# Kernel tuning notes

Hardware: AMD Instinct MI355X
Metric: run time of the kernel (lower is better)

Reference implementation:

```python
import jax, jax.numpy as jnp
import numpy as np

N_NODES = 100000
N_EDGES = 3200000
IN_DIM, HID_DIM, N_CLASS = 64, 32, 20


def setup_inputs() -> dict:
    key = jax.random.key(0)
    k1, k2, k3, k4, k5, k6 = jax.random.split(key, 6)
    x = jax.random.normal(k1, (N_NODES, IN_DIM), dtype=jnp.float32)
    edge_index = jax.random.randint(k2, (2, N_EDGES), 0, N_NODES, dtype=jnp.int64)
    W1 = jax.random.normal(k3, (IN_DIM, HID_DIM), dtype=jnp.float32) / np.sqrt(IN_DIM)
    b1 = jnp.zeros((HID_DIM,), dtype=jnp.float32)
    Wout = jax.random.normal(k4, (HID_DIM, N_CLASS), dtype=jnp.float32) / np.sqrt(HID_DIM)
    bout = jnp.zeros((N_CLASS,), dtype=jnp.float32)
    return {"x": x, "edge_index": edge_index, "W1": W1, "b1": b1, "Wout": Wout, "bout": bout}


def gcn_conv(x, edge_index, W, b):
    # PyG GCNConv defaults: add self-loops, symmetric deg^{-1/2} normalization.
    n = x.shape[0]
    loop = jnp.arange(n, dtype=edge_index.dtype)
    row = jnp.concatenate([edge_index[0], loop])  # source
    col = jnp.concatenate([edge_index[1], loop])  # target
    deg = jax.ops.segment_sum(jnp.ones_like(col, dtype=x.dtype), col, num_segments=n)
    dis = jnp.where(deg > 0, deg ** -0.5, 0.0)
    norm = dis[row] * dis[col]  # [E+N]
    xw = x @ W  # [N, HID]
    msg = norm[:, None] * xw[row]  # [E+N, HID]
    agg = jax.ops.segment_sum(msg, col, num_segments=n)
    return agg + b


def reference(x, edge_index, W1, b1, Wout, bout):
    h = gcn_conv(x, edge_index, W1, b1)
    emb = jax.nn.relu(h)
    return emb @ Wout + bout
```

## Files before the change

kernel.cpp:

```cpp
#include <hip/hip_runtime.h>
#include <hip/hip_fp16.h>
#include <math.h>

#define N_NODES 100000
#define N_EDGES 3200000
#define IN_DIM 64
#define HID_DIM 32
#define N_CLASS 20

#define BKT_BITS 6
#define BKT_W    64
#define NBKT     1563
#define CAP_BKT  2560
#define ENT_R    (CAP_BKT / 512)

#define SUP_SHIFT 12
#define SUP_W    (1 << SUP_SHIFT)
#define NS       25
#define CAP_S    132000
#define CH1      2048
#define NBLK1    ((N_EDGES + CH1 - 1) / CH1)
#define CH2      4096
#define BPS      ((CAP_S + CH2 - 1) / CH2)

__device__ __forceinline__ int get_idx(const int* __restrict__ ei32, int wide, int pos) {
    return wide ? ei32[2 * (long long)pos] : ei32[pos];
}

__global__ void __launch_bounds__(512, 4)
kS1(const int* __restrict__ ei32, int* __restrict__ scursor, unsigned int* __restrict__ sp) {
    __shared__ int lh[NS], lgb[NS], lrt[NS];
    __shared__ int sAny;
    if (threadIdx.x == 0) sAny = 0;
    if (threadIdx.x < NS) { lh[threadIdx.x] = 0; lrt[threadIdx.x] = 0; }
    int base = blockIdx.x * CH1;
    int e0 = base + (int)threadIdx.x;
    int probe = (e0 < N_EDGES) ? ei32[2 * (long long)e0 + 1] : 0;
    __syncthreads();
    if (probe) sAny = 1;
    __syncthreads();
    int wide = (sAny == 0);

    int src[4], dst[4];
#pragma unroll
    for (int k = 0; k < 4; ++k) {
        int e = base + k * 512 + (int)threadIdx.x;
        if (e < N_EDGES) {
            src[k] = get_idx(ei32, wide, e);
            dst[k] = get_idx(ei32, wide, N_EDGES + e);
            atomicAdd(&lh[dst[k] >> SUP_SHIFT], 1);
        } else dst[k] = -1;
    }
    __syncthreads();
    if (threadIdx.x < NS && lh[threadIdx.x])
        lgb[threadIdx.x] = atomicAdd(&scursor[threadIdx.x], lh[threadIdx.x]);
    __syncthreads();
#pragma unroll
    for (int k = 0; k < 4; ++k) {
        if (dst[k] >= 0) {
            int s = dst[k] >> SUP_SHIFT;
            int r = atomicAdd(&lrt[s], 1);
            int rel = lgb[s] + r;
            if (rel < CAP_S)
                sp[(size_t)s * CAP_S + rel] = ((unsigned)src[k] << SUP_SHIFT) |
                                              (unsigned)(dst[k] & (SUP_W - 1));
        }
    }
}

__global__ void __launch_bounds__(512, 4)
kS2(const unsigned int* __restrict__ sp, const int* __restrict__ scursor,
    int* __restrict__ gcursor, unsigned int* __restrict__ pk, int* __restrict__ deg) {
    __shared__ int lh[BKT_W], lgb[BKT_W], lrt[BKT_W];
    __shared__ int ndeg[SUP_W];
    int s = blockIdx.x / BPS;
    int j = blockIdx.x % BPS;
    int sbase = s * CAP_S;
    int scount = min(scursor[s], CAP_S);
    int start = j * CH2;
    if (start >= scount) return;
    int end = min(start + CH2, scount);
    for (int i = threadIdx.x; i < SUP_W; i += 512) ndeg[i] = 0;
    if (threadIdx.x < BKT_W) { lh[threadIdx.x] = 0; lrt[threadIdx.x] = 0; }
    __syncthreads();
    unsigned ent[8]; int fb[8];
#pragma unroll
    for (int k = 0; k < 8; ++k) {
        int i = start + k * 512 + (int)threadIdx.x;
        if (i < end) {
            ent[k] = sp[sbase + i];
            int ld = (int)(ent[k] & (SUP_W - 1));
            fb[k] = ld >> BKT_BITS;
            atomicAdd(&lh[fb[k]], 1);
            atomicAdd(&ndeg[ld], 1);
        } else fb[k] = -1;
    }
    __syncthreads();
    if (threadIdx.x < BKT_W && lh[threadIdx.x]) {
        int b = s * BKT_W + (int)threadIdx.x;
        if (b < NBKT) lgb[threadIdx.x] = atomicAdd(&gcursor[b], lh[threadIdx.x]);
    }
    __syncthreads();
#pragma unroll
    for (int k = 0; k < 8; ++k) {
        if (fb[k] >= 0) {
            int b = s * BKT_W + fb[k];
            int r = atomicAdd(&lrt[fb[k]], 1);
            int rel = lgb[fb[k]] + r;
            if (rel < CAP_BKT)
                pk[(size_t)b * CAP_BKT + rel] =
                    ((ent[k] >> SUP_SHIFT) << BKT_BITS) | (ent[k] & (BKT_W - 1));
        }
    }
    __syncthreads();
    int nodebase = s << SUP_SHIFT;
    for (int i = threadIdx.x; i < SUP_W; i += 512) {
        int c = ndeg[i];
        if (c && nodebase + i < N_NODES) atomicAdd(&deg[nodebase + i], c);
    }
}

__global__ void k_xw(const float* __restrict__ x, const float* __restrict__ W1,
                     const int* __restrict__ deg, __half* __restrict__ xw16) {
    __shared__ float sW[IN_DIM * HID_DIM];
    for (int i = threadIdx.x; i < IN_DIM * HID_DIM; i += blockDim.x) sW[i] = W1[i];
    __syncthreads();
    int tid = blockIdx.x * blockDim.x + threadIdx.x;
    int node = tid >> 3;
    int q = tid & 7;
    if (node >= N_NODES) return;
    const float4* xr = reinterpret_cast<const float4*>(x + (size_t)node * IN_DIM);
    float4 a = make_float4(0.f, 0.f, 0.f, 0.f);
#pragma unroll
    for (int k4 = 0; k4 < IN_DIM / 4; ++k4) {
        float4 xv = xr[k4];
        const float4 w0 = *reinterpret_cast<const float4*>(&sW[(k4 * 4 + 0) * HID_DIM + q * 4]);
        const float4 w1 = *reinterpret_cast<const float4*>(&sW[(k4 * 4 + 1) * HID_DIM + q * 4]);
        const float4 w2 = *reinterpret_cast<const float4*>(&sW[(k4 * 4 + 2) * HID_DIM + q * 4]);
        const float4 w3 = *reinterpret_cast<const float4*>(&sW[(k4 * 4 + 3) * HID_DIM + q * 4]);
        a.x += xv.x * w0.x + xv.y * w1.x + xv.z * w2.x + xv.w * w3.x;
        a.y += xv.x * w0.y + xv.y * w1.y + xv.z * w2.y + xv.w * w3.y;
        a.z += xv.x * w0.z + xv.y * w1.z + xv.z * w2.z + xv.w * w3.z;
        a.w += xv.x * w0.w + xv.y * w1.w + xv.z * w2.w + xv.w * w3.w;
    }
    float d = rsqrtf((float)(deg[node] + 1));
    union { __half2 h2[2]; uint2 u; } cvt;
    cvt.h2[0] = __floats2half2_rn(a.x * d, a.y * d);
    cvt.h2[1] = __floats2half2_rn(a.z * d, a.w * d);
    *reinterpret_cast<uint2*>(xw16 + (size_t)node * HID_DIM + q * 4) = cvt.u;
}

__device__ __forceinline__ void acc_row(float4& acc, uint2 u) {
    union U { unsigned u; __half2 hh; };
    U a0; a0.u = u.x; U a1; a1.u = u.y;
    float2 f0 = __half22float2(a0.hh);
    float2 f1 = __half22float2(a1.hh);
    acc.x += f0.x; acc.y += f0.y; acc.z += f1.x; acc.w += f1.y;
}

__global__ void __launch_bounds__(512, 8)
kD_gather(const unsigned int* __restrict__ pk, const int* __restrict__ gcursor,
          const int* __restrict__ deg, const __half* __restrict__ xw16,
          const float* __restrict__ b1, const float* __restrict__ Wout,
          const float* __restrict__ bout, float* __restrict__ out) {
    __shared__ int   ssrc[CAP_BKT];
    __shared__ int   lcnt[BKT_W], lstart[BKT_W], lrt[BKT_W];
    __shared__ float sW[HID_DIM * N_CLASS];
    __shared__ float sb1[HID_DIM];
    __shared__ float sbo[N_CLASS];
    for (int i = threadIdx.x; i < HID_DIM * N_CLASS; i += blockDim.x) sW[i] = Wout[i];
    if (threadIdx.x < HID_DIM) sb1[threadIdx.x] = b1[threadIdx.x];
    if (threadIdx.x < N_CLASS) sbo[threadIdx.x] = bout[threadIdx.x];
    if (threadIdx.x < BKT_W) lrt[threadIdx.x] = 0;
    int b = blockIdx.x;
    size_t gb = (size_t)b * CAP_BKT;
    int bsz = min(gcursor[b], CAP_BKT);
    if (threadIdx.x < BKT_W) {
        int node = b * BKT_W + (int)threadIdx.x;
        int v = (node < N_NODES) ? deg[node] : 0;
        lcnt[threadIdx.x] = v;
        int s = v;
#pragma unroll
        for (int d = 1; d < BKT_W; d <<= 1) {
            int t = __shfl_up(s, d, BKT_W);
            if ((int)threadIdx.x >= d) s += t;
        }
        lstart[threadIdx.x] = s - v;
    }
    __syncthreads();
    unsigned ents[ENT_R];
#pragma unroll
    for (int i = 0; i < ENT_R; ++i) {
        int idx = i * 512 + (int)threadIdx.x;
        ents[i] = (idx < bsz) ? pk[gb + idx] : 0xFFFFFFFFu;
    }
#pragma unroll
    for (int i = 0; i < ENT_R; ++i) {
        if (ents[i] != 0xFFFFFFFFu) {
            int ld = (int)(ents[i] & (BKT_W - 1));
            int r = atomicAdd(&lrt[ld], 1);
            int pos = lstart[ld] + r;
            if (pos < CAP_BKT) ssrc[pos] = (int)(ents[i] >> BKT_BITS);
        }
    }
    __syncthreads();

    int grp = threadIdx.x >> 3, part = threadIdx.x & 7;
    int node = b * BKT_W + grp;
    if (node >= N_NODES) return;

    float4 acc = make_float4(0.f, 0.f, 0.f, 0.f);
    acc_row(acc, *reinterpret_cast<const uint2*>(xw16 + (size_t)node * HID_DIM + part * 4));
    float dc = rsqrtf((float)(lcnt[grp] + 1));

    {
        int e = lstart[grp], end = min(lstart[grp] + lcnt[grp], CAP_BKT);
        while (e + 8 <= end) {
            uint2 us[8];
#pragma unroll
            for (int j = 0; j < 8; ++j)
                us[j] = *reinterpret_cast<const uint2*>(xw16 + (size_t)ssrc[e + j] * HID_DIM + part * 4);
#pragma unroll
            for (int j = 0; j < 8; ++j) acc_row(acc, us[j]);
            e += 8;
        }
        for (; e < end; ++e)
            acc_row(acc, *reinterpret_cast<const uint2*>(xw16 + (size_t)ssrc[e] * HID_DIM + part * 4));
    }
    float e0 = fmaxf(dc * acc.x + sb1[part * 4 + 0], 0.f);
    float e1 = fmaxf(dc * acc.y + sb1[part * 4 + 1], 0.f);
    float e2 = fmaxf(dc * acc.z + sb1[part * 4 + 2], 0.f);
    float e3 = fmaxf(dc * acc.w + sb1[part * 4 + 3], 0.f);
    float o[N_CLASS];
#pragma unroll
    for (int cl = 0; cl < N_CLASS; ++cl) {
        o[cl] = e0 * sW[(part * 4 + 0) * N_CLASS + cl]
              + e1 * sW[(part * 4 + 1) * N_CLASS + cl]
              + e2 * sW[(part * 4 + 2) * N_CLASS + cl]
              + e3 * sW[(part * 4 + 3) * N_CLASS + cl];
    }
#pragma unroll
    for (int m = 1; m < 8; m <<= 1) {
#pragma unroll
        for (int cl = 0; cl < N_CLASS; ++cl) o[cl] += __shfl_xor(o[cl], m, 64);
    }
    if (part < 5) {
        float4 w = make_float4(o[part * 4 + 0] + sbo[part * 4 + 0],
                               o[part * 4 + 1] + sbo[part * 4 + 1],
                               o[part * 4 + 2] + sbo[part * 4 + 2],
                               o[part * 4 + 3] + sbo[part * 4 + 3]);
        *reinterpret_cast<float4*>(out + (size_t)node * N_CLASS + part * 4) = w;
    }
}

extern "C" void kernel_launch(void* const* d_in, const int* in_sizes, int n_in,
                              void* d_out, int out_size, void* d_ws, size_t ws_size,
                              hipStream_t stream) {
    const float* x    = (const float*)d_in[0];
    const int*   ei32 = (const int*)d_in[1];
    const float* W1   = (const float*)d_in[2];
    const float* b1   = (const float*)d_in[3];
    const float* Wout = (const float*)d_in[4];
    const float* bout = (const float*)d_in[5];
    float* out = (float*)d_out;

    unsigned int* sp      = (unsigned int*)d_ws;
    __half*       xw16    = (__half*)d_ws;
    unsigned int* pk      = sp + (size_t)NS * CAP_S;
    int*          gcursor = (int*)(pk + (size_t)NBKT * CAP_BKT);
    int*          scursor = gcursor + NBKT;
    int*          deg     = scursor + NS;

    hipMemsetAsync(gcursor, 0, (size_t)(NBKT + NS + N_NODES) * sizeof(int), stream);

    kS1<<<NBLK1, 512, 0, stream>>>(ei32, scursor, sp);
    kS2<<<NS * BPS, 512, 0, stream>>>(sp, scursor, gcursor, pk, deg);
    k_xw<<<(N_NODES * 8 + 255) / 256, 256, 0, stream>>>(x, W1, deg, xw16);
    kD_gather<<<NBKT, 512, 0, stream>>>(pk, gcursor, deg, xw16, b1, Wout, bout, out);
}
```

Before: 128.1 us.

## Split fp16 XW into two 16-column slices and halve edge lists per lane group

The fp16 XW table is stored as two separate 16-column arrays, each 3.2 MB instead of one 6.4 MB array, so each gather pass works over a smaller footprint that fits caches better. Each node's 8 lanes are split into two halves that each process half the neighbor list over one slice, then combine with a shuffle, and the kernel makes two passes, one per slice. Bucket-entry loads and output stores use nontemporal hints. In exchange, every source index is read twice from LDS, and the row segments fetched per edge are narrower.

Measured after the change: 139.2 us. 1.09x slower.

```diff
diff --git a/kernel.cpp b/kernel.cpp
--- a/kernel.cpp
+++ b/kernel.cpp
@@ -7,6 +7,7 @@
 #define IN_DIM 64
 #define HID_DIM 32
 #define N_CLASS 20
+#define SLICE 16
 
 #define BKT_BITS 6
 #define BKT_W    64
@@ -121,7 +122,8 @@
 }
 
 __global__ void k_xw(const float* __restrict__ x, const float* __restrict__ W1,
-                     const int* __restrict__ deg, __half* __restrict__ xw16) {
+                     const int* __restrict__ deg, __half* __restrict__ xwA,
+                     __half* __restrict__ xwB) {
     __shared__ float sW[IN_DIM * HID_DIM];
     for (int i = threadIdx.x; i < IN_DIM * HID_DIM; i += blockDim.x) sW[i] = W1[i];
     __syncthreads();
@@ -147,7 +149,9 @@
     union { __half2 h2[2]; uint2 u; } cvt;
     cvt.h2[0] = __floats2half2_rn(a.x * d, a.y * d);
     cvt.h2[1] = __floats2half2_rn(a.z * d, a.w * d);
-    *reinterpret_cast<uint2*>(xw16 + (size_t)node * HID_DIM + q * 4) = cvt.u;
+    __half* dst = (q < 4) ? (xwA + (size_t)node * SLICE + q * 4)
+                          : (xwB + (size_t)node * SLICE + (q - 4) * 4);
+    *reinterpret_cast<uint2*>(dst) = cvt.u;
 }
 
 __device__ __forceinline__ void acc_row(float4& acc, uint2 u) {
@@ -158,11 +162,31 @@
     acc.x += f0.x; acc.y += f0.y; acc.z += f1.x; acc.w += f1.y;
 }
 
+__device__ __forceinline__ float4 gather_slice(const __half* __restrict__ xws,
+                                               const int* __restrict__ ssrc,
+                                               int beg, int end, int p) {
+    float4 acc = make_float4(0.f, 0.f, 0.f, 0.f);
+    int e = beg;
+    while (e + 8 <= end) {
+        uint2 us[8];
+#pragma unroll
+        for (int j = 0; j < 8; ++j)
+            us[j] = *reinterpret_cast<const uint2*>(xws + (size_t)ssrc[e + j] * SLICE + p * 4);
+#pragma unroll
+        for (int j = 0; j < 8; ++j) acc_row(acc, us[j]);
+        e += 8;
+    }
+    for (; e < end; ++e)
+        acc_row(acc, *reinterpret_cast<const uint2*>(xws + (size_t)ssrc[e] * SLICE + p * 4));
+    return acc;
+}
+
 __global__ void __launch_bounds__(512, 8)
 kD_gather(const unsigned int* __restrict__ pk, const int* __restrict__ gcursor,
-          const int* __restrict__ deg, const __half* __restrict__ xw16,
-          const float* __restrict__ b1, const float* __restrict__ Wout,
-          const float* __restrict__ bout, float* __restrict__ out) {
+          const int* __restrict__ deg, const __half* __restrict__ xwA,
+          const __half* __restrict__ xwB, const float* __restrict__ b1,
+          const float* __restrict__ Wout, const float* __restrict__ bout,
+          float* __restrict__ out) {
     __shared__ int   ssrc[CAP_BKT];
     __shared__ int   lcnt[BKT_W], lstart[BKT_W], lrt[BKT_W];
     __shared__ float sW[HID_DIM * N_CLASS];
@@ -192,7 +216,7 @@
 #pragma unroll
     for (int i = 0; i < ENT_R; ++i) {
         int idx = i * 512 + (int)threadIdx.x;
-        ents[i] = (idx < bsz) ? pk[gb + idx] : 0xFFFFFFFFu;
+        ents[i] = (idx < bsz) ? __builtin_nontemporal_load(pk + gb + idx) : 0xFFFFFFFFu;
     }
 #pragma unroll
     for (int i = 0; i < ENT_R; ++i) {
@@ -205,51 +229,60 @@
     }
     __syncthreads();
 
-    int grp = threadIdx.x >> 3, part = threadIdx.x & 7;
+    int grp = threadIdx.x >> 3;
+    int part = threadIdx.x & 7;
+    int p = part & 3;
+    int h = part >> 2;
     int node = b * BKT_W + grp;
     if (node >= N_NODES) return;
 
-    float4 acc = make_float4(0.f, 0.f, 0.f, 0.f);
-    acc_row(acc, *reinterpret_cast<const uint2*>(xw16 + (size_t)node * HID_DIM + part * 4));
-    float dc = rsqrtf((float)(lcnt[grp] + 1));
-
-    {
-        int e = lstart[grp], end = min(lstart[grp] + lcnt[grp], CAP_BKT);
-        while (e + 8 <= end) {
-            uint2 us[8];
-#pragma unroll
-            for (int j = 0; j < 8; ++j)
-                us[j] = *reinterpret_cast<const uint2*>(xw16 + (size_t)ssrc[e + j] * HID_DIM + part * 4);
-#pragma unroll
-            for (int j = 0; j < 8; ++j) acc_row(acc, us[j]);
-            e += 8;
-        }
-        for (; e < end; ++e)
-            acc_row(acc, *reinterpret_cast<const uint2*>(xw16 + (size_t)ssrc[e] * HID_DIM + part * 4));
-    }
-    float e0 = fmaxf(dc * acc.x + sb1[part * 4 + 0], 0.f);
-    float e1 = fmaxf(dc * acc.y + sb1[part * 4 + 1], 0.f);
-    float e2 = fmaxf(dc * acc.z + sb1[part * 4 + 2], 0.f);
-    float e3 = fmaxf(dc * acc.w + sb1[part * 4 + 3], 0.f);
+    int cnt = lcnt[grp], s0 = lstart[grp];
+    int m = (cnt + 1) >> 1;
+    int beg = s0 + (h ? m : 0);
+    int end = s0 + (h ? cnt : m);
+    float dc = rsqrtf((float)(cnt + 1));
+
+    float4 acc = gather_slice(xwA, ssrc, beg, end, p);
+    acc.x += __shfl_xor(acc.x, 4, 64); acc.y += __shfl_xor(acc.y, 4, 64);
+    acc.z += __shfl_xor(acc.z, 4, 64); acc.w += __shfl_xor(acc.w, 4, 64);
+    acc_row(acc, *reinterpret_cast<const uint2*>(xwA + (size_t)node * SLICE + p * 4));
+    float eA0 = fmaxf(dc * acc.x + sb1[p * 4 + 0], 0.f);
+    float eA1 = fmaxf(dc * acc.y + sb1[p * 4 + 1], 0.f);
+    float eA2 = fmaxf(dc * acc.z + sb1[p * 4 + 2], 0.f);
+    float eA3 = fmaxf(dc * acc.w + sb1[p * 4 + 3], 0.f);
+
+    acc = gather_slice(xwB, ssrc, beg, end, p);
+    acc.x += __shfl_xor(acc.x, 4, 64); acc.y += __shfl_xor(acc.y, 4, 64);
+    acc.z += __shfl_xor(acc.z, 4, 64); acc.w += __shfl_xor(acc.w, 4, 64);
+    acc_row(acc, *reinterpret_cast<const uint2*>(xwB + (size_t)node * SLICE + p * 4));
+    float eB0 = fmaxf(dc * acc.x + sb1[SLICE + p * 4 + 0], 0.f);
+    float eB1 = fmaxf(dc * acc.y + sb1[SLICE + p * 4 + 1], 0.f);
+    float eB2 = fmaxf(dc * acc.z + sb1[SLICE + p * 4 + 2], 0.f);
+    float eB3 = fmaxf(dc * acc.w + sb1[SLICE + p * 4 + 3], 0.f);
+
     float o[N_CLASS];
 #pragma unroll
     for (int cl = 0; cl < N_CLASS; ++cl) {
-        o[cl] = e0 * sW[(part * 4 + 0) * N_CLASS + cl]
-              + e1 * sW[(part * 4 + 1) * N_CLASS + cl]
-              + e2 * sW[(part * 4 + 2) * N_CLASS + cl]
-              + e3 * sW[(part * 4 + 3) * N_CLASS + cl];
-    }
-#pragma unroll
-    for (int m = 1; m < 8; m <<= 1) {
-#pragma unroll
-        for (int cl = 0; cl < N_CLASS; ++cl) o[cl] += __shfl_xor(o[cl], m, 64);
+        o[cl] = eA0 * sW[(p * 4 + 0) * N_CLASS + cl]
+              + eA1 * sW[(p * 4 + 1) * N_CLASS + cl]
+              + eA2 * sW[(p * 4 + 2) * N_CLASS + cl]
+              + eA3 * sW[(p * 4 + 3) * N_CLASS + cl]
+              + eB0 * sW[(SLICE + p * 4 + 0) * N_CLASS + cl]
+              + eB1 * sW[(SLICE + p * 4 + 1) * N_CLASS + cl]
+              + eB2 * sW[(SLICE + p * 4 + 2) * N_CLASS + cl]
+              + eB3 * sW[(SLICE + p * 4 + 3) * N_CLASS + cl];
+    }
+#pragma unroll
+    for (int m2 = 1; m2 < 4; m2 <<= 1) {
+#pragma unroll
+        for (int cl = 0; cl < N_CLASS; ++cl) o[cl] += __shfl_xor(o[cl], m2, 64);
     }
     if (part < 5) {
-        float4 w = make_float4(o[part * 4 + 0] + sbo[part * 4 + 0],
-                               o[part * 4 + 1] + sbo[part * 4 + 1],
-                               o[part * 4 + 2] + sbo[part * 4 + 2],
-                               o[part * 4 + 3] + sbo[part * 4 + 3]);
-        *reinterpret_cast<float4*>(out + (size_t)node * N_CLASS + part * 4) = w;
+        float* op = out + (size_t)node * N_CLASS + part * 4;
+        __builtin_nontemporal_store(o[part * 4 + 0] + sbo[part * 4 + 0], op + 0);
+        __builtin_nontemporal_store(o[part * 4 + 1] + sbo[part * 4 + 1], op + 1);
+        __builtin_nontemporal_store(o[part * 4 + 2] + sbo[part * 4 + 2], op + 2);
+        __builtin_nontemporal_store(o[part * 4 + 3] + sbo[part * 4 + 3], op + 3);
     }
 }
 
@@ -265,16 +298,17 @@
     float* out = (float*)d_out;
 
     unsigned int* sp      = (unsigned int*)d_ws;
-    __half*       xw16    = (__half*)d_ws;
+    __half*       xwA     = (__half*)d_ws;
+    __half*       xwB     = xwA + (size_t)N_NODES * SLICE;
     unsigned int* pk      = sp + (size_t)NS * CAP_S;
     int*          gcursor = (int*)(pk + (size_t)NBKT * CAP_BKT);
     int*          scursor = gcursor + NBKT;
     int*          deg     = scursor + NS;
 
-    hipMemsetAsync(gcursor, 0, (size_t)(NBKT + NS + N_NODES) * sizeof(int), stream);
+    (void)hipMemsetAsync(gcursor, 0, (size_t)(NBKT + NS + N_NODES) * sizeof(int), stream);
 
     kS1<<<NBLK1, 512, 0, stream>>>(ei32, scursor, sp);
     kS2<<<NS * BPS, 512, 0, stream>>>(sp, scursor, gcursor, pk, deg);
-    k_xw<<<(N_NODES * 8 + 255) / 256, 256, 0, stream>>>(x, W1, deg, xw16);
-    kD_gather<<<NBKT, 512, 0, stream>>>(pk, gcursor, deg, xw16, b1, Wout, bout, out);
-}
+    k_xw<<<(N_NODES * 8 + 255) / 256, 256, 0, stream>>>(x, W1, deg, xwA, xwB);
+    kD_gather<<<NBKT, 512, 0, stream>>>(pk, gcursor, deg, xwA, xwB, b1, Wout, bout, out);
+}
```

## Split gather into two source-range passes for L2 locality of xw16 rows

Applied to the files above, without the earlier changes.

The gather kernel is split into two kernels. The first sorts each bucket's edges by source half (below or above RSPLIT), writes the sorted sources back to pk, and accumulates only low-half sources into a global fp32 partial buffer. The second accumulates high-half sources from pk, adds the partial, and runs the bias/ReLU/output projection. Each pass touches only half of the xw16 table, so the intent is better L2/cache hit rates for the random row gathers. The cost is an extra kernel launch, a write and read of a 100000x32 fp32 partial, a pk rewrite, and nontemporal loads and stores.

Measured after the change: 154.2 us. 1.2x slower.

```diff
diff --git a/kernel.cpp b/kernel.cpp
--- a/kernel.cpp
+++ b/kernel.cpp
@@ -7,6 +7,7 @@
 #define IN_DIM 64
 #define HID_DIM 32
 #define N_CLASS 20
+#define RSPLIT 50000
 
 #define BKT_BITS 6
 #define BKT_W    64
@@ -159,26 +160,101 @@
 }
 
 __global__ void __launch_bounds__(512, 8)
-kD_gather(const unsigned int* __restrict__ pk, const int* __restrict__ gcursor,
-          const int* __restrict__ deg, const __half* __restrict__ xw16,
-          const float* __restrict__ b1, const float* __restrict__ Wout,
-          const float* __restrict__ bout, float* __restrict__ out) {
-    __shared__ int   ssrc[CAP_BKT];
-    __shared__ int   lcnt[BKT_W], lstart[BKT_W], lrt[BKT_W];
+kD0(unsigned int* __restrict__ pk, const int* __restrict__ gcursor,
+    const int* __restrict__ deg, const __half* __restrict__ xw16,
+    float* __restrict__ acc_g, int* __restrict__ cnt0g) {
+    __shared__ int ssrc[CAP_BKT];
+    __shared__ int lcnt[BKT_W], lstart[BKT_W], lc0[BKT_W], lrt0[BKT_W], lrt1[BKT_W];
+    int b = blockIdx.x;
+    size_t gb = (size_t)b * CAP_BKT;
+    int bsz = min(gcursor[b], CAP_BKT);
+    if (threadIdx.x < BKT_W) { lc0[threadIdx.x] = 0; lrt0[threadIdx.x] = 0; lrt1[threadIdx.x] = 0; }
+    if (threadIdx.x < BKT_W) {
+        int node = b * BKT_W + (int)threadIdx.x;
+        int v = (node < N_NODES) ? deg[node] : 0;
+        lcnt[threadIdx.x] = v;
+        int s = v;
+#pragma unroll
+        for (int d = 1; d < BKT_W; d <<= 1) {
+            int t = __shfl_up(s, d, BKT_W);
+            if ((int)threadIdx.x >= d) s += t;
+        }
+        lstart[threadIdx.x] = s - v;
+    }
+    __syncthreads();
+    unsigned ents[ENT_R];
+#pragma unroll
+    for (int i = 0; i < ENT_R; ++i) {
+        int idx = i * 512 + (int)threadIdx.x;
+        ents[i] = (idx < bsz) ? __builtin_nontemporal_load(pk + gb + idx) : 0xFFFFFFFFu;
+    }
+#pragma unroll
+    for (int i = 0; i < ENT_R; ++i) {
+        if (ents[i] != 0xFFFFFFFFu) {
+            int src = (int)(ents[i] >> BKT_BITS);
+            if (src < RSPLIT) atomicAdd(&lc0[ents[i] & (BKT_W - 1)], 1);
+        }
+    }
+    __syncthreads();
+#pragma unroll
+    for (int i = 0; i < ENT_R; ++i) {
+        if (ents[i] != 0xFFFFFFFFu) {
+            int ld = (int)(ents[i] & (BKT_W - 1));
+            int src = (int)(ents[i] >> BKT_BITS);
+            int pos;
+            if (src < RSPLIT) pos = lstart[ld] + atomicAdd(&lrt0[ld], 1);
+            else              pos = lstart[ld] + lc0[ld] + atomicAdd(&lrt1[ld], 1);
+            if (pos < CAP_BKT) { ssrc[pos] = src; pk[gb + pos] = (unsigned)src; }
+        }
+    }
+    if (threadIdx.x < BKT_W) cnt0g[b * BKT_W + (int)threadIdx.x] = lc0[threadIdx.x];
+    __syncthreads();
+
+    int grp = threadIdx.x >> 3, part = threadIdx.x & 7;
+    int node = b * BKT_W + grp;
+    if (node >= N_NODES) return;
+
+    float4 acc = make_float4(0.f, 0.f, 0.f, 0.f);
+    int e = lstart[grp], end = min(lstart[grp] + lc0[grp], CAP_BKT);
+    while (e + 8 <= end) {
+        uint2 us[8];
+#pragma unroll
+        for (int j = 0; j < 8; ++j)
+            us[j] = *reinterpret_cast<const uint2*>(xw16 + (size_t)ssrc[e + j] * HID_DIM + part * 4);
+#pragma unroll
+        for (int j = 0; j < 8; ++j) acc_row(acc, us[j]);
+        e += 8;
+    }
+    for (; e < end; ++e)
+        acc_row(acc, *reinterpret_cast<const uint2*>(xw16 + (size_t)ssrc[e] * HID_DIM + part * 4));
+
+    float* ap = acc_g + (size_t)node * HID_DIM + part * 4;
+    __builtin_nontemporal_store(acc.x, ap + 0);
+    __builtin_nontemporal_store(acc.y, ap + 1);
+    __builtin_nontemporal_store(acc.z, ap + 2);
+    __builtin_nontemporal_store(acc.w, ap + 3);
+}
+
+__global__ void __launch_bounds__(512, 8)
+kD1(const unsigned int* __restrict__ pk, const int* __restrict__ gcursor,
+    const int* __restrict__ deg, const int* __restrict__ cnt0g,
+    const __half* __restrict__ xw16, const float* __restrict__ acc_g,
+    const float* __restrict__ b1, const float* __restrict__ Wout,
+    const float* __restrict__ bout, float* __restrict__ out) {
+    __shared__ int   lcnt[BKT_W], lstart[BKT_W], lc0[BKT_W];
     __shared__ float sW[HID_DIM * N_CLASS];
     __shared__ float sb1[HID_DIM];
     __shared__ float sbo[N_CLASS];
     for (int i = threadIdx.x; i < HID_DIM * N_CLASS; i += blockDim.x) sW[i] = Wout[i];
     if (threadIdx.x < HID_DIM) sb1[threadIdx.x] = b1[threadIdx.x];
     if (threadIdx.x < N_CLASS) sbo[threadIdx.x] = bout[threadIdx.x];
-    if (threadIdx.x < BKT_W) lrt[threadIdx.x] = 0;
     int b = blockIdx.x;
     size_t gb = (size_t)b * CAP_BKT;
-    int bsz = min(gcursor[b], CAP_BKT);
     if (threadIdx.x < BKT_W) {
         int node = b * BKT_W + (int)threadIdx.x;
         int v = (node < N_NODES) ? deg[node] : 0;
         lcnt[threadIdx.x] = v;
+        lc0[threadIdx.x] = cnt0g[b * BKT_W + (int)threadIdx.x];
         int s = v;
 #pragma unroll
         for (int d = 1; d < BKT_W; d <<= 1) {
@@ -188,45 +264,40 @@
         lstart[threadIdx.x] = s - v;
     }
     __syncthreads();
-    unsigned ents[ENT_R];
-#pragma unroll
-    for (int i = 0; i < ENT_R; ++i) {
-        int idx = i * 512 + (int)threadIdx.x;
-        ents[i] = (idx < bsz) ? pk[gb + idx] : 0xFFFFFFFFu;
-    }
-#pragma unroll
-    for (int i = 0; i < ENT_R; ++i) {
-        if (ents[i] != 0xFFFFFFFFu) {
-            int ld = (int)(ents[i] & (BKT_W - 1));
-            int r = atomicAdd(&lrt[ld], 1);
-            int pos = lstart[ld] + r;
-            if (pos < CAP_BKT) ssrc[pos] = (int)(ents[i] >> BKT_BITS);
-        }
-    }
-    __syncthreads();
 
     int grp = threadIdx.x >> 3, part = threadIdx.x & 7;
     int node = b * BKT_W + grp;
     if (node >= N_NODES) return;
 
     float4 acc = make_float4(0.f, 0.f, 0.f, 0.f);
+    int e = min(lstart[grp] + lc0[grp], CAP_BKT);
+    int end = min(lstart[grp] + lcnt[grp], CAP_BKT);
+    while (e + 8 <= end) {
+        int srcs[8];
+#pragma unroll
+        for (int j = 0; j < 8; ++j)
+            srcs[j] = (int)__builtin_nontemporal_load(pk + gb + e + j);
+        uint2 us[8];
+#pragma unroll
+        for (int j = 0; j < 8; ++j)
+            us[j] = *reinterpret_cast<const uint2*>(xw16 + (size_t)srcs[j] * HID_DIM + part * 4);
+#pragma unroll
+        for (int j = 0; j < 8; ++j) acc_row(acc, us[j]);
+        e += 8;
+    }
+    for (; e < end; ++e) {
+        int src = (int)__builtin_nontemporal_load(pk + gb + e);
+        acc_row(acc, *reinterpret_cast<const uint2*>(xw16 + (size_t)src * HID_DIM + part * 4));
+    }
+    {
+        const float* ap = acc_g + (size_t)node * HID_DIM + part * 4;
+        acc.x += __builtin_nontemporal_load(ap + 0);
+        acc.y += __builtin_nontemporal_load(ap + 1);
+        acc.z += __builtin_nontemporal_load(ap + 2);
+        acc.w += __builtin_nontemporal_load(ap + 3);
+    }
     acc_row(acc, *reinterpret_cast<const uint2*>(xw16 + (size_t)node * HID_DIM + part * 4));
     float dc = rsqrtf((float)(lcnt[grp] + 1));
-
-    {
-        int e = lstart[grp], end = min(lstart[grp] + lcnt[grp], CAP_BKT);
-        while (e + 8 <= end) {
-            uint2 us[8];
-#pragma unroll
-            for (int j = 0; j < 8; ++j)
-                us[j] = *reinterpret_cast<const uint2*>(xw16 + (size_t)ssrc[e + j] * HID_DIM + part * 4);
-#pragma unroll
-            for (int j = 0; j < 8; ++j) acc_row(acc, us[j]);
-            e += 8;
-        }
-        for (; e < end; ++e)
-            acc_row(acc, *reinterpret_cast<const uint2*>(xw16 + (size_t)ssrc[e] * HID_DIM + part * 4));
-    }
     float e0 = fmaxf(dc * acc.x + sb1[part * 4 + 0], 0.f);
     float e1 = fmaxf(dc * acc.y + sb1[part * 4 + 1], 0.f);
     float e2 = fmaxf(dc * acc.z + sb1[part * 4 + 2], 0.f);
@@ -245,11 +316,11 @@
         for (int cl = 0; cl < N_CLASS; ++cl) o[cl] += __shfl_xor(o[cl], m, 64);
     }
     if (part < 5) {
-        float4 w = make_float4(o[part * 4 + 0] + sbo[part * 4 + 0],
-                               o[part * 4 + 1] + sbo[part * 4 + 1],
-                               o[part * 4 + 2] + sbo[part * 4 + 2],
-                               o[part * 4 + 3] + sbo[part * 4 + 3]);
-        *reinterpret_cast<float4*>(out + (size_t)node * N_CLASS + part * 4) = w;
+        float* op = out + (size_t)node * N_CLASS + part * 4;
+        __builtin_nontemporal_store(o[part * 4 + 0] + sbo[part * 4 + 0], op + 0);
+        __builtin_nontemporal_store(o[part * 4 + 1] + sbo[part * 4 + 1], op + 1);
+        __builtin_nontemporal_store(o[part * 4 + 2] + sbo[part * 4 + 2], op + 2);
+        __builtin_nontemporal_store(o[part * 4 + 3] + sbo[part * 4 + 3], op + 3);
     }
 }
 
@@ -270,11 +341,14 @@
     int*          gcursor = (int*)(pk + (size_t)NBKT * CAP_BKT);
     int*          scursor = gcursor + NBKT;
     int*          deg     = scursor + NS;
-
-    hipMemsetAsync(gcursor, 0, (size_t)(NBKT + NS + N_NODES) * sizeof(int), stream);
+    int*          cnt0    = deg + N_NODES;
+    float*        acc_g   = (float*)(cnt0 + NBKT * BKT_W);
+
+    (void)hipMemsetAsync(gcursor, 0, (size_t)(NBKT + NS + N_NODES) * sizeof(int), stream);
 
     kS1<<<NBLK1, 512, 0, stream>>>(ei32, scursor, sp);
     kS2<<<NS * BPS, 512, 0, stream>>>(sp, scursor, gcursor, pk, deg);
     k_xw<<<(N_NODES * 8 + 255) / 256, 256, 0, stream>>>(x, W1, deg, xw16);
-    kD_gather<<<NBKT, 512, 0, stream>>>(pk, gcursor, deg, xw16, b1, Wout, bout, out);
-}
+    kD0<<<NBKT, 512, 0, stream>>>(pk, gcursor, deg, xw16, acc_g, cnt0);
+    kD1<<<NBKT, 512, 0, stream>>>(pk, gcursor, deg, cnt0, xw16, acc_g, b1, Wout, bout, out);
+}
```
